# Performance work log

Measured on AMD Instinct MI355X. Metric: run time of the kernel, lower is better.

## Reference

```python
import jax, jax.numpy as jnp
import numpy as np
import math

B, C, H, W = 8, 512, 32, 32
ENC = 1024
L2 = 64
NH = 8
GROUPS = 32
EPS = 1e-5

def group_norm(x, gamma, beta):
    # x: (B, C, L) GroupNorm with 32 groups (float32)
    b, c, l = x.shape
    xg = x.reshape(b, GROUPS, (c // GROUPS) * l)
    mean = xg.mean(-1, keepdims=True)
    var = xg.var(-1, keepdims=True)
    xn = ((xg - mean) * jax.lax.rsqrt(var + EPS)).reshape(b, c, l)
    return xn * gamma[None, :, None] + beta[None, :, None]

def conv1x1(w, bias, x):
    # conv_nd(1, in, out, 1): w (out, in), x (B, in, L) -> (B, out, L)
    return jnp.einsum('oc,bcl->bol', w, x) + bias[None, :, None]

def setup_inputs() -> dict:
    key = jax.random.key(0)
    ks = jax.random.split(key, 16)
    s = lambda fan_in: 1.0 / math.sqrt(fan_in)
    inp = {
        'x': jax.random.normal(ks[0], (B, C, H, W), jnp.float32),
        'xf_out': jax.random.normal(ks[1], (B, ENC, L2), jnp.float32),
        'obj_class_embedding': jax.random.normal(ks[2], (B, ENC, L2), jnp.float32),
        'obj_bbox_embedding': jax.random.normal(ks[3], (B, ENC, L2), jnp.float32),
        'image_patch_bbox_embedding': jax.random.normal(ks[4], (B, ENC, H * W), jnp.float32),
        'key_padding_mask': jax.random.bernoulli(ks[5], 0.3, (B, L2)),
        'qkv_w': jax.random.normal(ks[6], (3 * C, C), jnp.float32) * s(C),
        'qkv_b': jnp.zeros((3 * C,), jnp.float32),
        'g_qkv': jnp.ones((C,), jnp.float32),
        'b_qkv': jnp.zeros((C,), jnp.float32),
        'lc_w': jax.random.normal(ks[7], (2 * C, ENC), jnp.float32) * s(ENC),
        'lc_b': jnp.zeros((2 * C,), jnp.float32),
        'lp_w': jax.random.normal(ks[8], (C, ENC), jnp.float32) * s(ENC),
        'lp_b': jnp.zeros((C,), jnp.float32),
        'g_obj': jnp.ones((ENC,), jnp.float32),
        'b_obj': jnp.zeros((ENC,), jnp.float32),
        'g_lpos': jnp.ones((C,), jnp.float32),
        'b_lpos': jnp.zeros((C,), jnp.float32),
        'g_ipos': jnp.ones((C,), jnp.float32),
        'b_ipos': jnp.zeros((C,), jnp.float32),
        # proj_out is zero-initialized in the original (zero_module); use random
        # weights so the projection math is exercised non-trivially.
        'proj_w': jax.random.normal(ks[9], (C, C), jnp.float32) * s(C),
        'proj_b': jnp.zeros((C,), jnp.float32),
    }
    return inp

def reference(x, xf_out, obj_class_embedding, obj_bbox_embedding,
              image_patch_bbox_embedding, key_padding_mask,
              qkv_w, qkv_b, g_qkv, b_qkv, lc_w, lc_b, lp_w, lp_b,
              g_obj, b_obj, g_lpos, b_lpos, g_ipos, b_ipos, proj_w, proj_b):
    b, c, h, w = x.shape
    L1 = h * w
    d = C // NH
    xf = x.reshape(b, c, L1)

    qkv = conv1x1(qkv_w, qkv_b, group_norm(xf, g_qkv, b_qkv))  # (B, 3C, L1)
    q, k, v = jnp.split(qkv, 3, axis=1)
    q = q.reshape(b * NH, d, L1)
    k = k.reshape(b * NH, d, L1)
    v = v.reshape(b * NH, d, L1)

    ipp = group_norm(conv1x1(lp_w, lp_b, image_patch_bbox_embedding), g_ipos, b_ipos)
    ipp = ipp.reshape(b * NH, d, L1)

    q_img = jnp.concatenate([q, ipp], axis=1)  # (B*H, 2d, L1)
    k_img = jnp.concatenate([k, ipp], axis=1)

    lpe = group_norm(conv1x1(lp_w, lp_b, obj_bbox_embedding), g_lpos, b_lpos)
    lpe = lpe.reshape(b * NH, d, L2)

    lce = (xf_out + group_norm(obj_class_embedding, g_obj, b_obj)) / 2
    kl, vl = jnp.split(conv1x1(lc_w, lc_b, lce), 2, axis=1)
    kl = kl.reshape(b * NH, d, L2)
    vl = vl.reshape(b * NH, d, L2)
    k_layout = jnp.concatenate([kl, lpe], axis=1)  # (B*H, 2d, L2)

    k_mix = jnp.concatenate([k_img, k_layout], axis=2)  # (B*H, 2d, L1+L2)
    v_mix = jnp.concatenate([v, vl], axis=2)             # (B*H, d, L1+L2)

    mask = jnp.concatenate([jnp.zeros((b, L1), bool), key_padding_mask], axis=1)  # (B, L1+L2)

    scale = 1.0 / math.sqrt(math.sqrt(2 * C // NH))
    attn = jnp.einsum('bct,bcs->bts', q_img * scale, k_mix * scale)  # (B*H, L1, L1+L2)
    attn = attn.reshape(b, NH, L1, L1 + L2)
    attn = jnp.where(mask[:, None, None, :], -jnp.inf, attn)
    attn = jax.nn.softmax(attn.astype(jnp.float32), axis=-1).astype(attn.dtype)
    attn = attn.reshape(b * NH, L1, L1 + L2)

    out = jnp.einsum('bts,bcs->bct', attn, v_mix).reshape(b, C, L1)
    hproj = conv1x1(proj_w, proj_b, out)
    return (xf + hproj).reshape(b, c, h, w)
```

## Files before the change

kernel.cpp:

```cpp
#include <hip/hip_runtime.h>
#include <math.h>

#define NB 8
#define NC 512
#define NL1 1024
#define NL2 64
#define NLKV 1088
#define NENC 1024
#define EPSV 1e-5f
#define SCALE2 0.08838834764831845f
#define SCALE2Q 0.12752425f
#define DEFER_THR 11.5415603f

typedef _Float16 half8 __attribute__((ext_vector_type(8)));
typedef _Float16 half4 __attribute__((ext_vector_type(4)));
typedef __fp16 fp16x2 __attribute__((ext_vector_type(2)));
typedef float f32x4 __attribute__((ext_vector_type(4)));
typedef float f32x16 __attribute__((ext_vector_type(16)));
typedef unsigned int uint32x2 __attribute__((ext_vector_type(2)));

__device__ __forceinline__ void gload16(const _Float16* g, _Float16* l) {
  __builtin_amdgcn_global_load_lds(
      (const __attribute__((address_space(1))) void*)g,
      (__attribute__((address_space(3))) void*)l, 16, 0, 0);
}

__device__ __forceinline__ unsigned int pkrtz(float a, float b) {
  union { fp16x2 hh; unsigned int uu; } cv;
  cv.hh = __builtin_amdgcn_cvt_pkrtz(a, b);
  return cv.uu;
}

__device__ __forceinline__ float fast_exp2(float x) {
  return __builtin_amdgcn_exp2f(x);
}

__global__ __launch_bounds__(256) void k_init(
    const float* __restrict__ x, const float* __restrict__ obj,
    float* __restrict__ xm, float* __restrict__ xr,
    float* __restrict__ om, float* __restrict__ orr,
    const float* __restrict__ qkv_w, _Float16* __restrict__ w16qkv,
    const float* __restrict__ lp_w, _Float16* __restrict__ w16lp,
    const float* __restrict__ proj_w, _Float16* __restrict__ w16proj,
    const float* __restrict__ lc_w, _Float16* __restrict__ w16lc)
{
  int bid = blockIdx.x;
  if (bid < 512) {
    const float* p; float* meanp; float* rstdp; int n4, n, bg;
    if (bid < 256) {
      bg = bid;
      int b = bg >> 5, g = bg & 31;
      p = x + ((size_t)b * 512 + (size_t)g * 16) * 1024;
      n = 16 * 1024; meanp = xm; rstdp = xr;
    } else {
      bg = bid - 256;
      int b = bg >> 5, g = bg & 31;
      p = obj + ((size_t)b * 1024 + (size_t)g * 32) * 64;
      n = 32 * 64; meanp = om; rstdp = orr;
    }
    n4 = n >> 2;
    float s = 0.f, s2 = 0.f;
    for (int i = threadIdx.x; i < n4; i += 256) {
      float4 v = ((const float4*)p)[i];
      s += v.x + v.y + v.z + v.w;
      s2 += v.x * v.x + v.y * v.y + v.z * v.z + v.w * v.w;
    }
    #pragma unroll
    for (int o = 32; o > 0; o >>= 1) { s += __shfl_down(s, o); s2 += __shfl_down(s2, o); }
    __shared__ float rs[4], rq[4];
    int lane = threadIdx.x & 63, w = threadIdx.x >> 6;
    if (lane == 0) { rs[w] = s; rq[w] = s2; }
    __syncthreads();
    if (threadIdx.x == 0) {
      float S = rs[0] + rs[1] + rs[2] + rs[3];
      float Q = rq[0] + rq[1] + rq[2] + rq[3];
      float m = S / n;
      float v = Q / n - m * m;
      if (v < 0.f) v = 0.f;
      meanp[bg] = m;
      rstdp[bg] = rsqrtf(v + EPSV);
    }
  } else {
    int cb = bid - 512;
    const float* s; _Float16* d; int i4;
    if (cb < 768)        { s = qkv_w;  d = w16qkv;  i4 = cb * 256 + threadIdx.x; }
    else if (cb < 1280)  { s = lp_w;   d = w16lp;   i4 = (cb - 768) * 256 + threadIdx.x; }
    else if (cb < 1536)  { s = proj_w; d = w16proj; i4 = (cb - 1280) * 256 + threadIdx.x; }
    else                 { s = lc_w;   d = w16lc;   i4 = (cb - 1536) * 256 + threadIdx.x; }
    float4 v = *(const float4*)&s[(size_t)i4 * 4];
    half4 o; o.x = (_Float16)v.x; o.y = (_Float16)v.y; o.z = (_Float16)v.z; o.w = (_Float16)v.w;
    *(half4*)&d[(size_t)i4 * 4] = o;
  }
}

__global__ __launch_bounds__(256) void k_prep(
    const float* __restrict__ x, const float* __restrict__ xm, const float* __restrict__ xr,
    const float* __restrict__ g_qkv, const float* __restrict__ b_qkv, _Float16* __restrict__ xT,
    const float* __restrict__ ipbe, _Float16* __restrict__ ipbeT,
    const float* __restrict__ xf_out, const float* __restrict__ obj_class,
    const float* __restrict__ obj_bbox,
    const float* __restrict__ om, const float* __restrict__ orr,
    const float* __restrict__ g_obj, const float* __restrict__ b_obj,
    _Float16* __restrict__ lceT, _Float16* __restrict__ objT)
{
  __shared__ _Float16 tile[64][72];
  const int bid = blockIdx.x;
  const int tl = threadIdx.x & 63;
  if (bid < 1024) {
    const int tt = bid & 15, ct = (bid >> 4) & 7, b = bid >> 7;
    const int c0 = ct * 64, t0 = tt * 64;
    const int cp = threadIdx.x >> 6;
    #pragma unroll
    for (int i = 0; i < 16; i++) {
      int c = c0 + i * 4 + cp;
      float v = x[((size_t)b * NC + c) * NL1 + t0 + tl];
      int g = c >> 4;
      float ga = g_qkv[c] * xr[b * 32 + g];
      float be = b_qkv[c] - xm[b * 32 + g] * ga;
      tile[tl][i * 4 + cp] = (_Float16)(v * ga + be);
    }
    __syncthreads();
    int tr = threadIdx.x >> 2, c16 = (threadIdx.x & 3) * 16;
    _Float16* dst = xT + ((size_t)b * 1024 + t0 + tr) * 512 + c0 + c16;
    *(half8*)dst = *(half8*)&tile[tr][c16];
    *(half8*)(dst + 8) = *(half8*)&tile[tr][c16 + 8];
  } else if (bid < 3072) {
    const int e2 = bid - 1024;
    const int tt = e2 & 15, et = (e2 >> 4) & 15, b = e2 >> 8;
    const int e0 = et * 64, t0 = tt * 64;
    const int ep = threadIdx.x >> 6;
    #pragma unroll
    for (int i = 0; i < 16; i++) {
      int e = e0 + i * 4 + ep;
      tile[tl][i * 4 + ep] = (_Float16)ipbe[((size_t)b * 1024 + e) * 1024 + t0 + tl];
    }
    __syncthreads();
    int tr = threadIdx.x >> 2, c16 = (threadIdx.x & 3) * 16;
    _Float16* d = ipbeT + ((size_t)b * 1024 + t0 + tr) * 1024 + e0 + c16;
    *(half8*)d = *(half8*)&tile[tr][c16];
    *(half8*)(d + 8) = *(half8*)&tile[tr][c16 + 8];
  } else {
    const int e2 = bid - 3072;
    const int et = e2 & 15, which = (e2 >> 4) & 1, b = e2 >> 5;
    const int e0 = et * 64;
    const int ep = threadIdx.x >> 6;
    if (which == 0) {
      #pragma unroll
      for (int i = 0; i < 16; i++) {
        int e = e0 + i * 4 + ep;
        size_t idx = ((size_t)b * 1024 + e) * 64 + tl;
        int g = e >> 5;
        float xn = (obj_class[idx] - om[b * 32 + g]) * orr[b * 32 + g] * g_obj[e] + b_obj[e];
        tile[tl][i * 4 + ep] = (_Float16)(0.5f * (xf_out[idx] + xn));
      }
    } else {
      #pragma unroll
      for (int i = 0; i < 16; i++) {
        int e = e0 + i * 4 + ep;
        tile[tl][i * 4 + ep] = (_Float16)obj_bbox[((size_t)b * 1024 + e) * 64 + tl];
      }
    }
    __syncthreads();
    int tr = threadIdx.x >> 2, c16 = (threadIdx.x & 3) * 16;
    _Float16* dst = (which == 0 ? lceT : objT) + ((size_t)b * 64 + tr) * 1024 + e0 + c16;
    *(half8*)dst = *(half8*)&tile[tr][c16];
    *(half8*)(dst + 8) = *(half8*)&tile[tr][c16 + 8];
  }
}

#define MFMA_CORE(KTOT)                                                                  \
  f32x4 acc[4][4];                                                                       \
  _Pragma("unroll") for (int i_ = 0; i_ < 4; i_++)                                       \
      _Pragma("unroll") for (int j_ = 0; j_ < 4; j_++) acc[i_][j_] = (f32x4)0.f;         \
  {                                                                                      \
    const int rsub = lane >> 3, csrc = (lane & 7) ^ rsub;                                \
    const int NT_ = (KTOT) / 64;                                                         \
    _Pragma("unroll") for (int i = 0; i < 4; i++) {                                      \
      int seg = w * 4 + i;                                                               \
      int row = seg * 8 + rsub;                                                          \
      gload16(Abase + (size_t)(m0 + row) * (KTOT) + csrc * 8, ldsA + seg * 512);         \
      gload16(Bbase + (size_t)(n0 + row) * (KTOT) + csrc * 8, ldsB + seg * 512);         \
    }                                                                                    \
    int cur_ = 0;                                                                        \
    for (int t_ = 0; t_ < NT_; t_++) {                                                   \
      if (t_ + 1 < NT_) {                                                                \
        _Float16* da_ = ldsA + ((cur_ ^ 1) << 13);                                       \
        _Float16* db_ = ldsB + ((cur_ ^ 1) << 13);                                       \
        int kt = (t_ + 1) * 64;                                                          \
        _Pragma("unroll") for (int i = 0; i < 4; i++) {                                  \
          int seg = w * 4 + i;                                                           \
          int row = seg * 8 + rsub;                                                      \
          gload16(Abase + (size_t)(m0 + row) * (KTOT) + kt + csrc * 8, da_ + seg * 512); \
          gload16(Bbase + (size_t)(n0 + row) * (KTOT) + kt + csrc * 8, db_ + seg * 512); \
        }                                                                                \
        asm volatile("s_waitcnt vmcnt(8)" ::: "memory");                                 \
      } else {                                                                           \
        asm volatile("s_waitcnt vmcnt(0)" ::: "memory");                                 \
      }                                                                                  \
      __builtin_amdgcn_s_barrier();                                                      \
      const char* ra_ = (const char*)(ldsA + (cur_ << 13));                              \
      const char* rb_ = (const char*)(ldsB + (cur_ << 13));                              \
      _Pragma("unroll") for (int kk = 0; kk < 2; kk++) {                                 \
        half8 af[4], bf[4];                                                              \
        _Pragma("unroll") for (int mb = 0; mb < 4; mb++) {                               \
          int row = wm + mb * 16 + l15;                                                  \
          af[mb] = *(const half8*)(ra_ + row * 128 +                                     \
                                   ((kk * 64 + lg * 16) ^ ((row & 7) << 4)));            \
        }                                                                                \
        _Pragma("unroll") for (int nb = 0; nb < 4; nb++) {                               \
          int row = wn + nb * 16 + l15;                                                  \
          bf[nb] = *(const half8*)(rb_ + row * 128 +                                     \
                                   ((kk * 64 + lg * 16) ^ ((row & 7) << 4)));            \
        }                                                                                \
        _Pragma("unroll") for (int mb = 0; mb < 4; mb++)                                 \
            _Pragma("unroll") for (int nb = 0; nb < 4; nb++)                             \
                acc[mb][nb] = __builtin_amdgcn_mfma_f32_16x16x32_f16(af[mb], bf[nb],     \
                                                                    acc[mb][nb], 0, 0, 0);\
      }                                                                                  \
      __builtin_amdgcn_s_barrier();                                                      \
      cur_ ^= 1;                                                                         \
    }                                                                                    \
  }

#define MFMA_CORE_N64(KTOT)                                                              \
  f32x4 acc[4][2];                                                                       \
  _Pragma("unroll") for (int i_ = 0; i_ < 4; i_++)                                       \
      _Pragma("unroll") for (int j_ = 0; j_ < 2; j_++) acc[i_][j_] = (f32x4)0.f;         \
  {                                                                                      \
    const int rsub = lane >> 3, csrc = (lane & 7) ^ rsub;                                \
    const int NT_ = (KTOT) / 64;                                                         \
    _Pragma("unroll") for (int i = 0; i < 4; i++) {                                      \
      int seg = w * 4 + i;                                                               \
      int row = seg * 8 + rsub;                                                          \
      gload16(Abase + (size_t)(m0 + row) * (KTOT) + csrc * 8, ldsA + seg * 512);         \
    }                                                                                    \
    _Pragma("unroll") for (int i = 0; i < 2; i++) {                                      \
      int seg = w * 2 + i;                                                               \
      int row = seg * 8 + rsub;                                                          \
      gload16(Bbase + (size_t)row * (KTOT) + csrc * 8, ldsB + seg * 512);                \
    }                                                                                    \
    int cur_ = 0;                                                                        \
    for (int t_ = 0; t_ < NT_; t_++) {                                                   \
      if (t_ + 1 < NT_) {                                                                \
        _Float16* da_ = ldsA + ((cur_ ^ 1) << 13);                                       \
        _Float16* db_ = ldsB + ((cur_ ^ 1) << 12);                                       \
        int kt = (t_ + 1) * 64;                                                          \
        _Pragma("unroll") for (int i = 0; i < 4; i++) {                                  \
          int seg = w * 4 + i;                                                           \
          int row = seg * 8 + rsub;                                                      \
          gload16(Abase + (size_t)(m0 + row) * (KTOT) + kt + csrc * 8, da_ + seg * 512); \
        }                                                                                \
        _Pragma("unroll") for (int i = 0; i < 2; i++) {                                  \
          int seg = w * 2 + i;                                                           \
          int row = seg * 8 + rsub;                                                      \
          gload16(Bbase + (size_t)row * (KTOT) + kt + csrc * 8, db_ + seg * 512);        \
        }                                                                                \
        asm volatile("s_waitcnt vmcnt(6)" ::: "memory");                                 \
      } else {                                                                           \
        asm volatile("s_waitcnt vmcnt(0)" ::: "memory");                                 \
      }                                                                                  \
      __builtin_amdgcn_s_barrier();                                                      \
      const char* ra_ = (const char*)(ldsA + (cur_ << 13));                              \
      const char* rb_ = (const char*)(ldsB + (cur_ << 12));                              \
      _Pragma("unroll") for (int kk = 0; kk < 2; kk++) {                                 \
        half8 af[4], bf[2];                                                              \
        _Pragma("unroll") for (int mb = 0; mb < 4; mb++) {                               \
          int row = wm + mb * 16 + l15;                                                  \
          af[mb] = *(const half8*)(ra_ + row * 128 +                                     \
                                   ((kk * 64 + lg * 16) ^ ((row & 7) << 4)));            \
        }                                                                                \
        _Pragma("unroll") for (int nb = 0; nb < 2; nb++) {                               \
          int row = wn + nb * 16 + l15;                                                  \
          bf[nb] = *(const half8*)(rb_ + row * 128 +                                     \
                                   ((kk * 64 + lg * 16) ^ ((row & 7) << 4)));            \
        }                                                                                \
        _Pragma("unroll") for (int mb = 0; mb < 4; mb++)                                 \
            _Pragma("unroll") for (int nb = 0; nb < 2; nb++)                             \
                acc[mb][nb] = __builtin_amdgcn_mfma_f32_16x16x32_f16(af[mb], bf[nb],     \
                                                                    acc[mb][nb], 0, 0, 0);\
      }                                                                                  \
      __builtin_amdgcn_s_barrier();                                                      \
      cur_ ^= 1;                                                                         \
    }                                                                                    \
  }

__global__ __launch_bounds__(256) void k_mfma_big(
    const _Float16* __restrict__ w16qkv, const float* __restrict__ qkv_b,
    const _Float16* __restrict__ xhatT,
    const _Float16* __restrict__ w16lp, const float* __restrict__ lp_b,
    const _Float16* __restrict__ ipbeT,
    const _Float16* __restrict__ w16lc, const float* __restrict__ lc_b,
    const _Float16* __restrict__ lceT, const _Float16* __restrict__ objT,
    const float* __restrict__ g_lpos, const float* __restrict__ b_lpos,
    _Float16* __restrict__ qT, _Float16* __restrict__ kT, _Float16* __restrict__ vT,
    _Float16* __restrict__ ipp16)
{
  __shared__ _Float16 smem[32768];
  const int bid0 = blockIdx.x;
  const int tid = threadIdx.x, lane = tid & 63, w = tid >> 6;
  const int l15 = lane & 15, lg = lane >> 4;

  if (bid0 < 256) {
    const int nt = bid0 & 7, mt = (bid0 >> 3) & 3, b = bid0 >> 5;
    const int m0 = mt * 128, n0 = nt * 128;
    _Float16* ldsA = smem;
    _Float16* ldsB = smem + 16384;
    const _Float16* Abase = w16lp;
    const _Float16* Bbase = ipbeT + (size_t)b * 1024 * 1024;
    const int wm = (w >> 1) * 64, wn = (w & 1) * 64;
    MFMA_CORE(1024)
    #pragma unroll
    for (int mb = 0; mb < 4; mb++) {
      #pragma unroll
      for (int r = 0; r < 4; r++) {
        int m = m0 + wm + mb * 16 + lg * 4 + r;
        float bia = lp_b[m];
        #pragma unroll
        for (int nb = 0; nb < 4; nb++) {
          int t = n0 + wn + nb * 16 + l15;
          ipp16[((size_t)b * NC + m) * NL1 + t] = (_Float16)(acc[mb][nb][r] + bia);
        }
      }
    }
  } else if (bid0 < 352) {
    const int local = bid0 - 256;
    const int mt = local % 12, b = local / 12;
    const bool islc = (mt < 8);
    const int m0 = (islc ? mt : mt - 8) * 128;
    _Float16* ldsA = smem;
    _Float16* ldsB = smem + 16384;
    float (*red_s)[4] = (float(*)[4])(smem + 24576);
    float (*red_q)[4] = (float(*)[4])(smem + 24608);
    const _Float16* Abase = islc ? w16lc : w16lp;
    const float* bias = islc ? lc_b : lp_b;
    const _Float16* Bbase = (islc ? lceT : objT) + (size_t)b * 64 * 1024;
    const int wm = (w >> 1) * 64, wn = (w & 1) * 32;
    MFMA_CORE_N64(1024)

    if (islc) {
      #pragma unroll
      for (int mb = 0; mb < 4; mb++) {
        #pragma unroll
        for (int r = 0; r < 4; r++) {
          int m = m0 + wm + mb * 16 + lg * 4 + r;
          float bia = bias[m];
          #pragma unroll
          for (int nb = 0; nb < 2; nb++) {
            int l = wn + nb * 16 + l15;
            float val = acc[mb][nb][r] + bia;
            if (m < 512) {
              int h = m >> 6, dc = m & 63;
              kT[(((size_t)b * 8 + h) * 1088 + 1024 + l) * 128 + dc] = (_Float16)val;
            } else {
              int mv = m - 512, h = mv >> 6, dc = mv & 63;
              vT[(((size_t)b * 8 + h) * 64 + dc) * 1088 + 1024 + l] = (_Float16)val;
            }
          }
        }
      }
    } else {
      float vals[4][2][4];
      float ps[4], pq[4];
      #pragma unroll
      for (int mb = 0; mb < 4; mb++) {
        ps[mb] = 0.f; pq[mb] = 0.f;
        #pragma unroll
        for (int r = 0; r < 4; r++) {
          int m = m0 + wm + mb * 16 + lg * 4 + r;
          float bia = bias[m];
          #pragma unroll
          for (int nb = 0; nb < 2; nb++) {
            float val = acc[mb][nb][r] + bia;
            vals[mb][nb][r] = val;
            ps[mb] += val; pq[mb] += val * val;
          }
        }
      }
      #pragma unroll
      for (int mb = 0; mb < 4; mb++) {
        #pragma unroll
        for (int o = 32; o > 0; o >>= 1) {
          ps[mb] += __shfl_xor(ps[mb], o);
          pq[mb] += __shfl_xor(pq[mb], o);
        }
      }
      if (lane == 0) {
        #pragma unroll
        for (int mb = 0; mb < 4; mb++) { red_s[w][mb] = ps[mb]; red_q[w][mb] = pq[mb]; }
      }
      __syncthreads();
      const int wbase = (wm >> 6) * 2;
      #pragma unroll
      for (int mb = 0; mb < 4; mb++) {
        float S = red_s[wbase][mb] + red_s[wbase + 1][mb];
        float Q = red_q[wbase][mb] + red_q[wbase + 1][mb];
        float mean = S * (1.f / 1024.f);
        float var = Q * (1.f / 1024.f) - mean * mean;
        if (var < 0.f) var = 0.f;
        float rstd = rsqrtf(var + EPSV);
        #pragma unroll
        for (int r = 0; r < 4; r++) {
          int c = m0 + wm + mb * 16 + lg * 4 + r;
          float ga = g_lpos[c] * rstd;
          float be = b_lpos[c] - mean * ga;
          int hh = c >> 6, dc = c & 63;
          #pragma unroll
          for (int nb = 0; nb < 2; nb++) {
            int l = wn + nb * 16 + l15;
            float xn = vals[mb][nb][r] * ga + be;
            kT[(((size_t)b * 8 + hh) * 1088 + 1024 + l) * 128 + 64 + dc] = (_Float16)xn;
          }
        }
      }
    }
  } else {
    const int bid = bid0 - 352;
    const int nt = bid & 7, tt = bid >> 3;
    const int mt = tt % 12, b = tt / 12;
    const int m0 = mt * 128, n0 = nt * 128;
    _Float16* ldsA = smem;
    _Float16* ldsB = smem + 16384;
    const _Float16* Abase = w16qkv;
    const _Float16* Bbase = xhatT + (size_t)b * 1024 * 512;
    const int wm = (w >> 1) * 64, wn = (w & 1) * 64;
    MFMA_CORE(512)

    char* tb = (char*)smem;
    if (m0 < 1024) {
      const bool isq = (m0 < 512);
      const float qs = isq ? SCALE2Q : 1.f;
      #pragma unroll
      for (int mb = 0; mb < 4; mb++) {
        #pragma unroll
        for (int r = 0; r < 4; r++) {
          int mcol = wm + mb * 16 + lg * 4 + r;
          float bia = qkv_b[m0 + mcol];
          #pragma unroll
          for (int nb = 0; nb < 4; nb++) {
            int trow = wn + nb * 16 + l15;
            float val = (acc[mb][nb][r] + bia) * qs;
            *(_Float16*)(tb + ((trow * 256 + mcol * 2) ^ ((trow & 7) << 4))) = (_Float16)val;
          }
        }
      }
      __syncthreads();
      #pragma unroll
      for (int it = 0; it < 8; it++) {
        int e = it * 256 + tid;
        int trow = e >> 4, seg = e & 15;
        half8 v = *(const half8*)(tb + ((trow * 256 + seg * 16) ^ ((trow & 7) << 4)));
        if (isq) {
          int mq = m0 + seg * 8, hh = mq >> 6, dc = mq & 63;
          *(half8*)(qT + (((size_t)b * 8 + hh) * 1024 + n0 + trow) * 128 + dc) = v;
        } else {
          int mk = m0 - 512 + seg * 8, hh = mk >> 6, dc = mk & 63;
          *(half8*)(kT + (((size_t)b * 8 + hh) * 1088 + n0 + trow) * 128 + dc) = v;
        }
      }
    } else {
      #pragma unroll
      for (int mb = 0; mb < 4; mb++) {
        #pragma unroll
        for (int r = 0; r < 4; r++) {
          int mrow = wm + mb * 16 + lg * 4 + r;
          float bia = qkv_b[m0 + mrow];
          #pragma unroll
          for (int nb = 0; nb < 4; nb++) {
            int tcol = wn + nb * 16 + l15;
            *(_Float16*)(tb + ((mrow * 256 + tcol * 2) ^ ((mrow & 7) << 4))) =
                (_Float16)(acc[mb][nb][r] + bia);
          }
        }
      }
      __syncthreads();
      #pragma unroll
      for (int it = 0; it < 8; it++) {
        int e = it * 256 + tid;
        int mrow = e >> 4, seg = e & 15;
        half8 v = *(const half8*)(tb + ((mrow * 256 + seg * 16) ^ ((mrow & 7) << 4)));
        int mv = m0 - 1024 + mrow, hh = mv >> 6, dc = mv & 63;
        *(half8*)(vT + (((size_t)b * 8 + hh) * 64 + dc) * 1088 + n0 + seg * 8) = v;
      }
    }
  }
}

__global__ __launch_bounds__(256) void k_mfma_proj(
    const _Float16* __restrict__ Abase, const float* __restrict__ bias,
    const _Float16* __restrict__ Ball, const float* __restrict__ xin,
    float* __restrict__ out)
{
  __shared__ _Float16 smem[32768];
  _Float16* ldsA = smem;
  _Float16* ldsB = smem + 16384;
  const int b = blockIdx.z, mt = blockIdx.y, nt = blockIdx.x;
  const int m0 = mt * 128, n0 = nt * 128;
  const _Float16* Bbase = Ball + (size_t)b * 1024 * 512;
  const int tid = threadIdx.x, lane = tid & 63, w = tid >> 6;
  const int l15 = lane & 15, lg = lane >> 4;
  const int wm = (w >> 1) * 64, wn = (w & 1) * 64;
  MFMA_CORE(512)
  #pragma unroll
  for (int mb = 0; mb < 4; mb++) {
    #pragma unroll
    for (int r = 0; r < 4; r++) {
      int m = m0 + wm + mb * 16 + lg * 4 + r;
      float bia = bias[m];
      #pragma unroll
      for (int nb = 0; nb < 4; nb++) {
        int t = n0 + wn + nb * 16 + l15;
        size_t idx = ((size_t)b * NC + m) * NL1 + t;
        out[idx] = xin[idx] + acc[mb][nb][r] + bia;
      }
    }
  }
}

__global__ __launch_bounds__(256) void k_ipp_fuse(
    const _Float16* __restrict__ raw,
    const float* __restrict__ gm, const float* __restrict__ gb,
    _Float16* __restrict__ qT, _Float16* __restrict__ kT)
{
  const int g = blockIdx.x, b = blockIdx.y;
  const int tid = threadIdx.x;
  const _Float16* p = raw + ((size_t)b * 512 + (size_t)g * 16) * 1024;
  const int t0 = tid * 4;

  float4 v[16];
  float s = 0.f, s2 = 0.f;
  #pragma unroll
  for (int c = 0; c < 16; c++) {
    half4 hv = *(const half4*)&p[(size_t)c * 1024 + t0];
    v[c].x = (float)hv.x; v[c].y = (float)hv.y; v[c].z = (float)hv.z; v[c].w = (float)hv.w;
    s += v[c].x + v[c].y + v[c].z + v[c].w;
    s2 += v[c].x * v[c].x + v[c].y * v[c].y + v[c].z * v[c].z + v[c].w * v[c].w;
  }
  #pragma unroll
  for (int o = 32; o > 0; o >>= 1) { s += __shfl_down(s, o); s2 += __shfl_down(s2, o); }
  __shared__ float rs[4], rq[4], stat[2];
  int lane = tid & 63, w = tid >> 6;
  if (lane == 0) { rs[w] = s; rq[w] = s2; }
  __syncthreads();
  if (tid == 0) {
    float S = rs[0] + rs[1] + rs[2] + rs[3];
    float Q = rq[0] + rq[1] + rq[2] + rq[3];
    float mn = S / 16384.f;
    float var = Q / 16384.f - mn * mn;
    if (var < 0.f) var = 0.f;
    stat[0] = mn; stat[1] = rsqrtf(var + EPSV);
  }
  __syncthreads();
  const float mn = stat[0], rstd = stat[1];

  float ga[16], be[16];
  #pragma unroll
  for (int c = 0; c < 16; c++) {
    ga[c] = gm[g * 16 + c] * rstd;
    be[c] = gb[g * 16 + c] - mn * ga[c];
  }

  const size_t bh = (size_t)b * 8 + (g >> 2);
  const int dcb = (g & 3) * 16;
  #pragma unroll
  for (int j = 0; j < 4; j++) {
    const int t = t0 + j;
    half8 k0, k1, q0, q1;
    #pragma unroll
    for (int c = 0; c < 8; c++) {
      float4 vc = v[c];
      float e = (j == 0) ? vc.x : (j == 1) ? vc.y : (j == 2) ? vc.z : vc.w;
      float xn = e * ga[c] + be[c];
      k0[c] = (_Float16)xn;
      q0[c] = (_Float16)(SCALE2Q * xn);
    }
    #pragma unroll
    for (int c = 8; c < 16; c++) {
      float4 vc = v[c];
      float e = (j == 0) ? vc.x : (j == 1) ? vc.y : (j == 2) ? vc.z : vc.w;
      float xn = e * ga[c] + be[c];
      k1[c - 8] = (_Float16)xn;
      q1[c - 8] = (_Float16)(SCALE2Q * xn);
    }
    _Float16* qd = qT + (bh * 1024 + t) * 128 + 64 + dcb;
    _Float16* kd = kT + (bh * 1088 + t) * 128 + 64 + dcb;
    *(half8*)qd = q0; *(half8*)(qd + 8) = q1;
    *(half8*)kd = k0; *(half8*)(kd + 8) = k1;
  }
}

__global__ __launch_bounds__(512, 1) void k_attn_mfma(
    const _Float16* __restrict__ qT, const _Float16* __restrict__ kT,
    const _Float16* __restrict__ vT, const int* __restrict__ mask,
    _Float16* __restrict__ attnT)
{
  const int bid = blockIdx.x;
  const int bh = bid & 63;
  const int qt = bid >> 6;
  const int b = bh >> 3, h = bh & 7;
  const int tid = threadIdx.x;
  const int lane = tid & 63;
  const int w = tid >> 6;
  const int l31 = lane & 31;
  const int hi = lane >> 5;

  __shared__ _Float16 KsB[2 * 64 * 128];
  __shared__ _Float16 VtB[3 * 64 * 64];

  const int q = qt * 256 + w * 32 + l31;

  half8 aq[8];
  {
    const _Float16* qp = qT + ((size_t)bh * 1024 + q) * 128 + hi * 8;
    #pragma unroll
    for (int kst = 0; kst < 8; kst++) aq[kst] = *(const half8*)(qp + kst * 16);
  }

  unsigned int mbits = 0;
  {
    const int* mp = mask + b * 64;
    #pragma unroll
    for (int sb = 0; sb < 2; sb++) {
      #pragma unroll
      for (int reg = 0; reg < 16; reg++) {
        int s = sb * 32 + (reg & 3) + 8 * (reg >> 2) + 4 * hi;
        if (mp[s]) mbits |= 1u << (sb * 16 + reg);
      }
    }
  }

  f32x16 O0 = (f32x16)0.f, O1 = (f32x16)0.f;
  f32x16 scA0 = (f32x16)0.f, scA1 = (f32x16)0.f;
  f32x16 scB0 = (f32x16)0.f, scB1 = (f32x16)0.f;
  float m_run = -INFINITY, l_run = 0.f;

  const int kxor = (l31 & 7) << 4;
  const int ksrow_off = lane >> 4;
  const int kcsrc_base = lane & 15;
  const int vdc_off = lane >> 3;
  const int vcsrc_base = lane & 7;

#define STAGE_KV(T, KD, VD)                                                          \
  {                                                                                  \
    const int s0_ = (T) * 64;                                                        \
    _Pragma("unroll") for (int r = 0; r < 2; r++) {                                  \
      int seg = r * 8 + w;                                                           \
      int srow = seg * 4 + ksrow_off;                                                \
      int csrc = kcsrc_base ^ (srow & 7);                                            \
      gload16(kT + ((size_t)bh * 1088 + s0_ + srow) * 128 + csrc * 8, (KD) + seg * 512); \
    }                                                                                \
    {                                                                                \
      int seg = w;                                                                   \
      int dc = seg * 8 + vdc_off;                                                    \
      int csrc = vcsrc_base ^ (dc & 7);                                              \
      gload16(vT + ((size_t)bh * 64 + dc) * 1088 + s0_ + csrc * 8, (VD) + seg * 512);  \
    }                                                                                \
  }

#define XHALF_FMAX(OUTV, INV)                                                        \
  { unsigned int xi_ = __float_as_uint(INV);                                         \
    uint32x2 xr_ = __builtin_amdgcn_permlane32_swap(xi_, xi_, false, false);         \
    OUTV = fmaxf(__uint_as_float(xr_.x), __uint_as_float(xr_.y)); }
#define XHALF_ADD(OUTV, INV)                                                         \
  { unsigned int xi_ = __float_as_uint(INV);                                         \
    uint32x2 xr_ = __builtin_amdgcn_permlane32_swap(xi_, xi_, false, false);         \
    OUTV = __uint_as_float(xr_.x) + __uint_as_float(xr_.y); }

#define ATTN_ITER(C0, C1, P0, P1, T)                                                 \
  {                                                                                  \
    const int T_ = (T);                                                              \
    if (T_ <= 16) {                                                                  \
      if (T_ <= 15) {                                                                \
        _Float16* kd_ = KsB + (((T_ + 1) & 1) << 13);                                \
        _Float16* vd_ = VtB + ((T_ + 1) % 3) * 4096;                                 \
        STAGE_KV(T_ + 1, kd_, vd_)                                                   \
      }                                                                              \
      const char* ksb_ = (const char*)(KsB + ((T_ & 1) << 13));                      \
      C0 = (f32x16)0.f; C1 = (f32x16)0.f;                                            \
      __builtin_amdgcn_s_setprio(1);                                                 \
      _Pragma("unroll") for (int kst = 0; kst < 8; kst++) {                          \
        half8 kf0 = *(const half8*)(ksb_ + ((l31 * 256 + kst * 32 + hi * 16) ^ kxor)); \
        half8 kf1 = *(const half8*)(ksb_ + (((32 + l31) * 256 + kst * 32 + hi * 16) ^ kxor)); \
        C0 = __builtin_amdgcn_mfma_f32_32x32x16_f16(kf0, aq[kst], C0, 0, 0, 0);      \
        C1 = __builtin_amdgcn_mfma_f32_32x32x16_f16(kf1, aq[kst], C1, 0, 0, 0);      \
      }                                                                              \
      __builtin_amdgcn_s_setprio(0);                                                 \
    }                                                                                \
    if (T_ >= 1) {                                                                   \
      if (T_ == 17) {                                                                \
        _Pragma("unroll") for (int i = 0; i < 16; i++) {                             \
          if ((mbits >> i) & 1)        P0[i] = -INFINITY;                            \
          if ((mbits >> (16 + i)) & 1) P1[i] = -INFINITY;                            \
        }                                                                            \
      }                                                                              \
      float mx;                                                                      \
      {                                                                              \
        float a0 = fmaxf(fmaxf(P0[0], P0[1]), P0[2]);                                \
        float a1 = fmaxf(fmaxf(P0[3], P0[4]), P0[5]);                                \
        float a2 = fmaxf(fmaxf(P0[6], P0[7]), P0[8]);                                \
        float a3 = fmaxf(fmaxf(P0[9], P0[10]), P0[11]);                              \
        float a4 = fmaxf(fmaxf(P0[12], P0[13]), P0[14]);                             \
        float a5 = fmaxf(fmaxf(P0[15], P1[0]), P1[1]);                               \
        float a6 = fmaxf(fmaxf(P1[2], P1[3]), P1[4]);                                \
        float a7 = fmaxf(fmaxf(P1[5], P1[6]), P1[7]);                                \
        float a8 = fmaxf(fmaxf(P1[8], P1[9]), P1[10]);                               \
        float a9 = fmaxf(fmaxf(P1[11], P1[12]), P1[13]);                             \
        float aa = fmaxf(P1[14], P1[15]);                                            \
        float b0 = fmaxf(fmaxf(a0, a1), a2);                                         \
        float b1 = fmaxf(fmaxf(a3, a4), a5);                                         \
        float b2 = fmaxf(fmaxf(a6, a7), a8);                                         \
        float b3 = fmaxf(a9, aa);                                                    \
        mx = fmaxf(fmaxf(b0, b1), fmaxf(b2, b3));                                    \
      }                                                                              \
      XHALF_FMAX(mx, mx)                                                             \
      if (__all(mx <= m_run + DEFER_THR)) {                                          \
        float sum = 0.f;                                                             \
        _Pragma("unroll") for (int i = 0; i < 16; i++) {                             \
          float p = fast_exp2(P0[i] - m_run); P0[i] = p; sum += p; }                 \
        _Pragma("unroll") for (int i = 0; i < 16; i++) {                             \
          float p = fast_exp2(P1[i] - m_run); P1[i] = p; sum += p; }                 \
        XHALF_ADD(sum, sum)                                                          \
        l_run += sum;                                                                \
      } else {                                                                       \
        float m_new = fmaxf(m_run, mx);                                              \
        float alpha = fast_exp2(m_run - m_new);                                      \
        float sum = 0.f;                                                             \
        _Pragma("unroll") for (int i = 0; i < 16; i++) {                             \
          float p = fast_exp2(P0[i] - m_new); P0[i] = p; sum += p; }                 \
        _Pragma("unroll") for (int i = 0; i < 16; i++) {                             \
          float p = fast_exp2(P1[i] - m_new); P1[i] = p; sum += p; }                 \
        XHALF_ADD(sum, sum)                                                          \
        l_run = l_run * alpha + sum;                                                 \
        m_run = m_new;                                                               \
        _Pragma("unroll") for (int i = 0; i < 16; i++) { O0[i] *= alpha; O1[i] *= alpha; } \
      }                                                                              \
      const char* vtb_ = (const char*)(VtB + ((T_ - 1) % 3) * 4096);                 \
      __builtin_amdgcn_s_setprio(1);                                                 \
      _Pragma("unroll") for (int sb = 0; sb < 2; sb++) {                             \
        _Pragma("unroll") for (int k2 = 0; k2 < 2; k2++) {                           \
          const int kst = sb * 2 + k2;                                               \
          unsigned int pa0, pa1, pb0, pb1;                                           \
          if (sb == 0) {                                                             \
            pa0 = pkrtz(P0[8 * k2 + 0], P0[8 * k2 + 1]);                             \
            pa1 = pkrtz(P0[8 * k2 + 2], P0[8 * k2 + 3]);                             \
            pb0 = pkrtz(P0[8 * k2 + 4], P0[8 * k2 + 5]);                             \
            pb1 = pkrtz(P0[8 * k2 + 6], P0[8 * k2 + 7]);                             \
          } else {                                                                   \
            pa0 = pkrtz(P1[8 * k2 + 0], P1[8 * k2 + 1]);                             \
            pa1 = pkrtz(P1[8 * k2 + 2], P1[8 * k2 + 3]);                             \
            pb0 = pkrtz(P1[8 * k2 + 4], P1[8 * k2 + 5]);                             \
            pb1 = pkrtz(P1[8 * k2 + 6], P1[8 * k2 + 7]);                             \
          }                                                                          \
          uint32x2 r0_ = __builtin_amdgcn_permlane32_swap(pa0, pb0, false, false);   \
          uint32x2 r1_ = __builtin_amdgcn_permlane32_swap(pa1, pb1, false, false);   \
          union { unsigned int u[4]; half8 hh; } pf;                                 \
          pf.u[0] = r0_.x;                                                           \
          pf.u[1] = r1_.x;                                                           \
          pf.u[2] = r0_.y;                                                           \
          pf.u[3] = r1_.y;                                                           \
          half8 vf0 = *(const half8*)(vtb_ + ((l31 * 128 + kst * 32 + hi * 16) ^ kxor)); \
          half8 vf1 = *(const half8*)(vtb_ + (((32 + l31) * 128 + kst * 32 + hi * 16) ^ kxor)); \
          O0 = __builtin_amdgcn_mfma_f32_32x32x16_f16(vf0, pf.hh, O0, 0, 0, 0);      \
          O1 = __builtin_amdgcn_mfma_f32_32x32x16_f16(vf1, pf.hh, O1, 0, 0, 0);      \
        }                                                                            \
      }                                                                              \
      __builtin_amdgcn_s_setprio(0);                                                 \
    }                                                                                \
    if (T_ < 17) {                                                                   \
      asm volatile("s_waitcnt vmcnt(0)" ::: "memory");                               \
      __builtin_amdgcn_s_barrier();                                                  \
    }                                                                                \
  }

  STAGE_KV(0, KsB, VtB)
  asm volatile("s_waitcnt vmcnt(0)" ::: "memory");
  __builtin_amdgcn_s_barrier();

  for (int t = 0; t < 18; t += 2) {
    ATTN_ITER(scA0, scA1, scB0, scB1, t)
    ATTN_ITER(scB0, scB1, scA0, scA1, t + 1)
  }

  float inv = 1.f / l_run;
  _Float16* op = attnT + ((size_t)b * 1024 + q) * 512 + h * 64;
  #pragma unroll
  for (int i = 0; i < 16; i += 2) {
    int dc = (i & 3) + 8 * (i >> 2) + 4 * hi;
    unsigned int c0 = pkrtz(O0[i] * inv, O0[i + 1] * inv);
    unsigned int c1 = pkrtz(O1[i] * inv, O1[i + 1] * inv);
    *(unsigned int*)(op + dc) = c0;
    *(unsigned int*)(op + 32 + dc) = c1;
  }
}

extern "C" void kernel_launch(void* const* d_in, const int* in_sizes, int n_in,
                              void* d_out, int out_size, void* d_ws, size_t ws_size,
                              hipStream_t stream) {
  const float* x         = (const float*)d_in[0];
  const float* xf_out    = (const float*)d_in[1];
  const float* obj_class = (const float*)d_in[2];
  const float* obj_bbox  = (const float*)d_in[3];
  const float* ipbe      = (const float*)d_in[4];
  const int*   mask      = (const int*)d_in[5];
  const float* qkv_w     = (const float*)d_in[6];
  const float* qkv_b     = (const float*)d_in[7];
  const float* g_qkv     = (const float*)d_in[8];
  const float* b_qkv     = (const float*)d_in[9];
  const float* lc_w      = (const float*)d_in[10];
  const float* lc_b      = (const float*)d_in[11];
  const float* lp_w      = (const float*)d_in[12];
  const float* lp_b      = (const float*)d_in[13];
  const float* g_obj     = (const float*)d_in[14];
  const float* b_obj     = (const float*)d_in[15];
  const float* g_lpos    = (const float*)d_in[16];
  const float* b_lpos    = (const float*)d_in[17];
  const float* g_ipos    = (const float*)d_in[18];
  const float* b_ipos    = (const float*)d_in[19];
  const float* proj_w    = (const float*)d_in[20];
  const float* proj_b    = (const float*)d_in[21];
  float* out = (float*)d_out;

  _Float16* f16b = (_Float16*)d_ws;
  _Float16* qT      = f16b;
  _Float16* kT      = qT + 8388608;
  _Float16* vT      = kT + 8912896;
  _Float16* xhatT   = vT + 4456448;
  _Float16* ipbeT   = xhatT + 4194304;
  _Float16* attnT   = ipbeT + 8388608;
  _Float16* w16qkv  = attnT + 4194304;
  _Float16* w16lp   = w16qkv + 786432;
  _Float16* w16proj = w16lp + 524288;
  _Float16* w16lc   = w16proj + 262144;
  _Float16* lceT    = w16lc + 1048576;
  _Float16* objT    = lceT + 524288;
  _Float16* ipp16   = objT + 524288;
  float* st = (float*)(ipp16 + 4194304);
  float* xm = st, * xr = st + 256, * om = st + 512, * orr = st + 768;

  dim3 blk(256);
  k_init<<<dim3(3072), blk, 0, stream>>>(x, obj_class, xm, xr, om, orr,
                                         qkv_w, w16qkv, lp_w, w16lp, proj_w, w16proj, lc_w, w16lc);
  k_prep<<<dim3(3328), blk, 0, stream>>>(x, xm, xr, g_qkv, b_qkv, xhatT,
                                         ipbe, ipbeT,
                                         xf_out, obj_class, obj_bbox, om, orr, g_obj, b_obj,
                                         lceT, objT);
  k_mfma_big<<<dim3(1120), blk, 0, stream>>>(w16qkv, qkv_b, xhatT,
                                             w16lp, lp_b, ipbeT,
                                             w16lc, lc_b, lceT, objT,
                                             g_lpos, b_lpos,
                                             qT, kT, vT, ipp16);
  k_ipp_fuse<<<dim3(32, 8), blk, 0, stream>>>(ipp16, g_ipos, b_ipos, qT, kT);
  k_attn_mfma<<<dim3(256), dim3(512), 0, stream>>>(qT, kT, vT, mask, attnT);
  k_mfma_proj<<<dim3(8, 4, 8), blk, 0, stream>>>(w16proj, proj_b, attnT, x, out);
}
```

Baseline: 125.5 us.

## Enlarge big GEMM tiles to 256x256 with 512-thread blocks

The fused projection GEMM kernel moves from 128x128 tiles with 256 threads to 256x256 tiles with 512 threads and 128KB of LDS, cutting the grid from 1120 to 304 blocks. The small N=64 GEMMs pair two 128-row tiles per block, using the two halves of the block. Larger tiles raise operand reuse per LDS load and reduce redundant global reads. In exchange, each block uses more LDS and registers, and the epilogue transpose goes through two serialized passes with extra barriers. Fewer blocks may also leave some of the device's compute units idle.

```diff
diff --git a/kernel.cpp b/kernel.cpp
--- a/kernel.cpp
+++ b/kernel.cpp
@@ -168,9 +168,9 @@
   }
 }
 
-#define MFMA_CORE(KTOT)                                                                  \
-  f32x4 acc[4][4];                                                                       \
-  _Pragma("unroll") for (int i_ = 0; i_ < 4; i_++)                                       \
+#define MFMA_CORE_256(KTOT)                                                              \
+  f32x4 acc[8][4];                                                                       \
+  _Pragma("unroll") for (int i_ = 0; i_ < 8; i_++)                                       \
       _Pragma("unroll") for (int j_ = 0; j_ < 4; j_++) acc[i_][j_] = (f32x4)0.f;         \
   {                                                                                      \
     const int rsub = lane >> 3, csrc = (lane & 7) ^ rsub;                                \
@@ -184,8 +184,8 @@
     int cur_ = 0;                                                                        \
     for (int t_ = 0; t_ < NT_; t_++) {                                                   \
       if (t_ + 1 < NT_) {                                                                \
-        _Float16* da_ = ldsA + ((cur_ ^ 1) << 13);                                       \
-        _Float16* db_ = ldsB + ((cur_ ^ 1) << 13);                                       \
+        _Float16* da_ = ldsA + ((cur_ ^ 1) << 14);                                       \
+        _Float16* db_ = ldsB + ((cur_ ^ 1) << 14);                                       \
         int kt = (t_ + 1) * 64;                                                          \
         _Pragma("unroll") for (int i = 0; i < 4; i++) {                                  \
           int seg = w * 4 + i;                                                           \
@@ -198,11 +198,11 @@
         asm volatile("s_waitcnt vmcnt(0)" ::: "memory");                                 \
       }                                                                                  \
       __builtin_amdgcn_s_barrier();                                                      \
-      const char* ra_ = (const char*)(ldsA + (cur_ << 13));                              \
-      const char* rb_ = (const char*)(ldsB + (cur_ << 13));                              \
+      const char* ra_ = (const char*)(ldsA + (cur_ << 14));                              \
+      const char* rb_ = (const char*)(ldsB + (cur_ << 14));                              \
       _Pragma("unroll") for (int kk = 0; kk < 2; kk++) {                                 \
-        half8 af[4], bf[4];                                                              \
-        _Pragma("unroll") for (int mb = 0; mb < 4; mb++) {                               \
+        half8 af[8], bf[4];                                                              \
+        _Pragma("unroll") for (int mb = 0; mb < 8; mb++) {                               \
           int row = wm + mb * 16 + l15;                                                  \
           af[mb] = *(const half8*)(ra_ + row * 128 +                                     \
                                    ((kk * 64 + lg * 16) ^ ((row & 7) << 4)));            \
@@ -212,7 +212,7 @@
           bf[nb] = *(const half8*)(rb_ + row * 128 +                                     \
                                    ((kk * 64 + lg * 16) ^ ((row & 7) << 4)));            \
         }                                                                                \
-        _Pragma("unroll") for (int mb = 0; mb < 4; mb++)                                 \
+        _Pragma("unroll") for (int mb = 0; mb < 8; mb++)                                 \
             _Pragma("unroll") for (int nb = 0; nb < 4; nb++)                             \
                 acc[mb][nb] = __builtin_amdgcn_mfma_f32_16x16x32_f16(af[mb], bf[nb],     \
                                                                     acc[mb][nb], 0, 0, 0);\
@@ -284,7 +284,61 @@
     }                                                                                    \
   }
 
-__global__ __launch_bounds__(256) void k_mfma_big(
+#define MFMA_CORE(KTOT)                                                                  \
+  f32x4 acc[4][4];                                                                       \
+  _Pragma("unroll") for (int i_ = 0; i_ < 4; i_++)                                       \
+      _Pragma("unroll") for (int j_ = 0; j_ < 4; j_++) acc[i_][j_] = (f32x4)0.f;         \
+  {                                                                                      \
+    const int rsub = lane >> 3, csrc = (lane & 7) ^ rsub;                                \
+    const int NT_ = (KTOT) / 64;                                                         \
+    _Pragma("unroll") for (int i = 0; i < 4; i++) {                                      \
+      int seg = w * 4 + i;                                                               \
+      int row = seg * 8 + rsub;                                                          \
+      gload16(Abase + (size_t)(m0 + row) * (KTOT) + csrc * 8, ldsA + seg * 512);         \
+      gload16(Bbase + (size_t)(n0 + row) * (KTOT) + csrc * 8, ldsB + seg * 512);         \
+    }                                                                                    \
+    int cur_ = 0;                                                                        \
+    for (int t_ = 0; t_ < NT_; t_++) {                                                   \
+      if (t_ + 1 < NT_) {                                                                \
+        _Float16* da_ = ldsA + ((cur_ ^ 1) << 13);                                       \
+        _Float16* db_ = ldsB + ((cur_ ^ 1) << 13);                                       \
+        int kt = (t_ + 1) * 64;                                                          \
+        _Pragma("unroll") for (int i = 0; i < 4; i++) {                                  \
+          int seg = w * 4 + i;                                                           \
+          int row = seg * 8 + rsub;                                                      \
+          gload16(Abase + (size_t)(m0 + row) * (KTOT) + kt + csrc * 8, da_ + seg * 512); \
+          gload16(Bbase + (size_t)(n0 + row) * (KTOT) + kt + csrc * 8, db_ + seg * 512); \
+        }                                                                                \
+        asm volatile("s_waitcnt vmcnt(8)" ::: "memory");                                 \
+      } else {                                                                           \
+        asm volatile("s_waitcnt vmcnt(0)" ::: "memory");                                 \
+      }                                                                                  \
+      __builtin_amdgcn_s_barrier();                                                      \
+      const char* ra_ = (const char*)(ldsA + (cur_ << 13));                              \
+      const char* rb_ = (const char*)(ldsB + (cur_ << 13));                              \
+      _Pragma("unroll") for (int kk = 0; kk < 2; kk++) {                                 \
+        half8 af[4], bf[4];                                                              \
+        _Pragma("unroll") for (int mb = 0; mb < 4; mb++) {                               \
+          int row = wm + mb * 16 + l15;                                                  \
+          af[mb] = *(const half8*)(ra_ + row * 128 +                                     \
+                                   ((kk * 64 + lg * 16) ^ ((row & 7) << 4)));            \
+        }                                                                                \
+        _Pragma("unroll") for (int nb = 0; nb < 4; nb++) {                               \
+          int row = wn + nb * 16 + l15;                                                  \
+          bf[nb] = *(const half8*)(rb_ + row * 128 +                                     \
+                                   ((kk * 64 + lg * 16) ^ ((row & 7) << 4)));            \
+        }                                                                                \
+        _Pragma("unroll") for (int mb = 0; mb < 4; mb++)                                 \
+            _Pragma("unroll") for (int nb = 0; nb < 4; nb++)                             \
+                acc[mb][nb] = __builtin_amdgcn_mfma_f32_16x16x32_f16(af[mb], bf[nb],     \
+                                                                    acc[mb][nb], 0, 0, 0);\
+      }                                                                                  \
+      __builtin_amdgcn_s_barrier();                                                      \
+      cur_ ^= 1;                                                                         \
+    }                                                                                    \
+  }
+
+__global__ __launch_bounds__(512, 2) void k_mfma_big(
     const _Float16* __restrict__ w16qkv, const float* __restrict__ qkv_b,
     const _Float16* __restrict__ xhatT,
     const _Float16* __restrict__ w16lp, const float* __restrict__ lp_b,
@@ -295,22 +349,22 @@
     _Float16* __restrict__ qT, _Float16* __restrict__ kT, _Float16* __restrict__ vT,
     _Float16* __restrict__ ipp16)
 {
-  __shared__ _Float16 smem[32768];
+  __shared__ _Float16 smem[65536];
   const int bid0 = blockIdx.x;
   const int tid = threadIdx.x, lane = tid & 63, w = tid >> 6;
-  const int l15 = lane & 15, lg = lane >> 4;
-
-  if (bid0 < 256) {
-    const int nt = bid0 & 7, mt = (bid0 >> 3) & 3, b = bid0 >> 5;
-    const int m0 = mt * 128, n0 = nt * 128;
+  const int l15 = lane & 15, lg = (lane >> 4) & 3;
+
+  if (bid0 < 64) {
+    const int nt = bid0 & 3, mt = (bid0 >> 2) & 1, b = bid0 >> 3;
+    const int m0 = mt * 256, n0 = nt * 256;
     _Float16* ldsA = smem;
-    _Float16* ldsB = smem + 16384;
+    _Float16* ldsB = smem + 32768;
     const _Float16* Abase = w16lp;
     const _Float16* Bbase = ipbeT + (size_t)b * 1024 * 1024;
-    const int wm = (w >> 1) * 64, wn = (w & 1) * 64;
-    MFMA_CORE(1024)
+    const int wm = (w >> 2) * 128, wn = (w & 3) * 64;
+    MFMA_CORE_256(1024)
     #pragma unroll
-    for (int mb = 0; mb < 4; mb++) {
+    for (int mb = 0; mb < 8; mb++) {
       #pragma unroll
       for (int r = 0; r < 4; r++) {
         int m = m0 + wm + mb * 16 + lg * 4 + r;
@@ -322,164 +376,197 @@
         }
       }
     }
-  } else if (bid0 < 352) {
-    const int local = bid0 - 256;
-    const int mt = local % 12, b = local / 12;
-    const bool islc = (mt < 8);
-    const int m0 = (islc ? mt : mt - 8) * 128;
-    _Float16* ldsA = smem;
-    _Float16* ldsB = smem + 16384;
-    float (*red_s)[4] = (float(*)[4])(smem + 24576);
-    float (*red_q)[4] = (float(*)[4])(smem + 24608);
+  } else if (bid0 < 112) {
+    const int local = bid0 - 64;
+    const int j = local % 6, b = local / 6;
+    const int h = w >> 2;
+    const bool islc = (j < 4);
+    const int m0 = islc ? (j * 2 + h) * 128 : ((j - 4) * 2 + h) * 128;
+    _Float16* ldsA = smem + h * 24576;
+    _Float16* ldsB = smem + h * 24576 + 16384;
+    float (*red_s)[4] = (float(*)[4])((char*)smem + 98304);
+    float (*red_q)[4] = (float(*)[4])((char*)smem + 98304 + 128);
     const _Float16* Abase = islc ? w16lc : w16lp;
     const float* bias = islc ? lc_b : lp_b;
     const _Float16* Bbase = (islc ? lceT : objT) + (size_t)b * 64 * 1024;
-    const int wm = (w >> 1) * 64, wn = (w & 1) * 32;
-    MFMA_CORE_N64(1024)
-
-    if (islc) {
-      #pragma unroll
-      for (int mb = 0; mb < 4; mb++) {
+    {
+      const int w = (tid >> 6) & 3;
+      const int wm = (w >> 1) * 64, wn = (w & 1) * 32;
+      MFMA_CORE_N64(1024)
+
+      if (islc) {
         #pragma unroll
-        for (int r = 0; r < 4; r++) {
-          int m = m0 + wm + mb * 16 + lg * 4 + r;
-          float bia = bias[m];
+        for (int mb = 0; mb < 4; mb++) {
           #pragma unroll
-          for (int nb = 0; nb < 2; nb++) {
-            int l = wn + nb * 16 + l15;
-            float val = acc[mb][nb][r] + bia;
-            if (m < 512) {
-              int h = m >> 6, dc = m & 63;
-              kT[(((size_t)b * 8 + h) * 1088 + 1024 + l) * 128 + dc] = (_Float16)val;
-            } else {
-              int mv = m - 512, h = mv >> 6, dc = mv & 63;
-              vT[(((size_t)b * 8 + h) * 64 + dc) * 1088 + 1024 + l] = (_Float16)val;
+          for (int r = 0; r < 4; r++) {
+            int m = m0 + wm + mb * 16 + lg * 4 + r;
+            float bia = bias[m];
+            #pragma unroll
+            for (int nb = 0; nb < 2; nb++) {
+              int l = wn + nb * 16 + l15;
+              float val = acc[mb][nb][r] + bia;
+              if (m < 512) {
+                int hh = m >> 6, dc = m & 63;
+                kT[(((size_t)b * 8 + hh) * 1088 + 1024 + l) * 128 + dc] = (_Float16)val;
+              } else {
+                int mv = m - 512, hh = mv >> 6, dc = mv & 63;
+                vT[(((size_t)b * 8 + hh) * 64 + dc) * 1088 + 1024 + l] = (_Float16)val;
+              }
+            }
+          }
+        }
+      } else {
+        float vals[4][2][4];
+        float ps[4], pq[4];
+        #pragma unroll
+        for (int mb = 0; mb < 4; mb++) {
+          ps[mb] = 0.f; pq[mb] = 0.f;
+          #pragma unroll
+          for (int r = 0; r < 4; r++) {
+            int m = m0 + wm + mb * 16 + lg * 4 + r;
+            float bia = bias[m];
+            #pragma unroll
+            for (int nb = 0; nb < 2; nb++) {
+              float val = acc[mb][nb][r] + bia;
+              vals[mb][nb][r] = val;
+              ps[mb] += val; pq[mb] += val * val;
+            }
+          }
+        }
+        #pragma unroll
+        for (int mb = 0; mb < 4; mb++) {
+          #pragma unroll
+          for (int o = 32; o > 0; o >>= 1) {
+            ps[mb] += __shfl_xor(ps[mb], o);
+            pq[mb] += __shfl_xor(pq[mb], o);
+          }
+        }
+        if (lane == 0) {
+          #pragma unroll
+          for (int mb = 0; mb < 4; mb++) { red_s[h * 4 + w][mb] = ps[mb]; red_q[h * 4 + w][mb] = pq[mb]; }
+        }
+        __syncthreads();
+        const int wbase = h * 4 + (wm >> 6) * 2;
+        #pragma unroll
+        for (int mb = 0; mb < 4; mb++) {
+          float S = red_s[wbase][mb] + red_s[wbase + 1][mb];
+          float Q = red_q[wbase][mb] + red_q[wbase + 1][mb];
+          float mean = S * (1.f / 1024.f);
+          float var = Q * (1.f / 1024.f) - mean * mean;
+          if (var < 0.f) var = 0.f;
+          float rstd = rsqrtf(var + EPSV);
+          #pragma unroll
+          for (int r = 0; r < 4; r++) {
+            int c = m0 + wm + mb * 16 + lg * 4 + r;
+            float ga = g_lpos[c] * rstd;
+            float be = b_lpos[c] - mean * ga;
+            int hh = c >> 6, dc = c & 63;
+            #pragma unroll
+            for (int nb = 0; nb < 2; nb++) {
+              int l = wn + nb * 16 + l15;
+              float xn = vals[mb][nb][r] * ga + be;
+              kT[(((size_t)b * 8 + hh) * 1088 + 1024 + l) * 128 + 64 + dc] = (_Float16)xn;
             }
           }
         }
       }
-    } else {
-      float vals[4][2][4];
-      float ps[4], pq[4];
-      #pragma unroll
-      for (int mb = 0; mb < 4; mb++) {
-        ps[mb] = 0.f; pq[mb] = 0.f;
-        #pragma unroll
-        for (int r = 0; r < 4; r++) {
-          int m = m0 + wm + mb * 16 + lg * 4 + r;
-          float bia = bias[m];
-          #pragma unroll
-          for (int nb = 0; nb < 2; nb++) {
-            float val = acc[mb][nb][r] + bia;
-            vals[mb][nb][r] = val;
-            ps[mb] += val; pq[mb] += val * val;
-          }
-        }
-      }
-      #pragma unroll
-      for (int mb = 0; mb < 4; mb++) {
-        #pragma unroll
-        for (int o = 32; o > 0; o >>= 1) {
-          ps[mb] += __shfl_xor(ps[mb], o);
-          pq[mb] += __shfl_xor(pq[mb], o);
-        }
-      }
-      if (lane == 0) {
-        #pragma unroll
-        for (int mb = 0; mb < 4; mb++) { red_s[w][mb] = ps[mb]; red_q[w][mb] = pq[mb]; }
-      }
-      __syncthreads();
-      const int wbase = (wm >> 6) * 2;
-      #pragma unroll
-      for (int mb = 0; mb < 4; mb++) {
-        float S = red_s[wbase][mb] + red_s[wbase + 1][mb];
-        float Q = red_q[wbase][mb] + red_q[wbase + 1][mb];
-        float mean = S * (1.f / 1024.f);
-        float var = Q * (1.f / 1024.f) - mean * mean;
-        if (var < 0.f) var = 0.f;
-        float rstd = rsqrtf(var + EPSV);
-        #pragma unroll
-        for (int r = 0; r < 4; r++) {
-          int c = m0 + wm + mb * 16 + lg * 4 + r;
-          float ga = g_lpos[c] * rstd;
-          float be = b_lpos[c] - mean * ga;
-          int hh = c >> 6, dc = c & 63;
-          #pragma unroll
-          for (int nb = 0; nb < 2; nb++) {
-            int l = wn + nb * 16 + l15;
-            float xn = vals[mb][nb][r] * ga + be;
-            kT[(((size_t)b * 8 + hh) * 1088 + 1024 + l) * 128 + 64 + dc] = (_Float16)xn;
-          }
-        }
-      }
     }
   } else {
-    const int bid = bid0 - 352;
-    const int nt = bid & 7, tt = bid >> 3;
-    const int mt = tt % 12, b = tt / 12;
-    const int m0 = mt * 128, n0 = nt * 128;
+    const int local = bid0 - 112;
+    const int nt = local & 3, tt = local >> 2;
+    const int mt = tt % 6, b = tt / 6;
+    const int m0 = mt * 256, n0 = nt * 256;
     _Float16* ldsA = smem;
-    _Float16* ldsB = smem + 16384;
+    _Float16* ldsB = smem + 32768;
     const _Float16* Abase = w16qkv;
     const _Float16* Bbase = xhatT + (size_t)b * 1024 * 512;
-    const int wm = (w >> 1) * 64, wn = (w & 1) * 64;
-    MFMA_CORE(512)
+    const int wm = (w >> 2) * 128, wn = (w & 3) * 64;
+    MFMA_CORE_256(512)
 
     char* tb = (char*)smem;
+    const int mi_w = w >> 2;
+    const int ti_w = (w & 3) >> 1;
+    const int w1 = w & 1;
+
     if (m0 < 1024) {
       const bool isq = (m0 < 512);
       const float qs = isq ? SCALE2Q : 1.f;
       #pragma unroll
-      for (int mb = 0; mb < 4; mb++) {
-        #pragma unroll
-        for (int r = 0; r < 4; r++) {
-          int mcol = wm + mb * 16 + lg * 4 + r;
-          float bia = qkv_b[m0 + mcol];
+      for (int ti = 0; ti < 2; ti++) {
+        if (ti_w == ti) {
+          char* tbm = tb + mi_w * 32768;
           #pragma unroll
-          for (int nb = 0; nb < 4; nb++) {
-            int trow = wn + nb * 16 + l15;
-            float val = (acc[mb][nb][r] + bia) * qs;
-            *(_Float16*)(tb + ((trow * 256 + mcol * 2) ^ ((trow & 7) << 4))) = (_Float16)val;
+          for (int mb = 0; mb < 8; mb++) {
+            #pragma unroll
+            for (int r = 0; r < 4; r++) {
+              int mloc = mb * 16 + lg * 4 + r;
+              float bia = qkv_b[m0 + mi_w * 128 + mloc];
+              #pragma unroll
+              for (int nb = 0; nb < 4; nb++) {
+                int tloc = w1 * 64 + nb * 16 + l15;
+                float val = (acc[mb][nb][r] + bia) * qs;
+                *(_Float16*)(tbm + ((tloc * 256 + mloc * 2) ^ ((tloc & 7) << 4))) = (_Float16)val;
+              }
+            }
           }
         }
-      }
-      __syncthreads();
-      #pragma unroll
-      for (int it = 0; it < 8; it++) {
-        int e = it * 256 + tid;
-        int trow = e >> 4, seg = e & 15;
-        half8 v = *(const half8*)(tb + ((trow * 256 + seg * 16) ^ ((trow & 7) << 4)));
-        if (isq) {
-          int mq = m0 + seg * 8, hh = mq >> 6, dc = mq & 63;
-          *(half8*)(qT + (((size_t)b * 8 + hh) * 1024 + n0 + trow) * 128 + dc) = v;
-        } else {
-          int mk = m0 - 512 + seg * 8, hh = mk >> 6, dc = mk & 63;
-          *(half8*)(kT + (((size_t)b * 8 + hh) * 1088 + n0 + trow) * 128 + dc) = v;
+        __syncthreads();
+        #pragma unroll
+        for (int mi = 0; mi < 2; mi++) {
+          char* tbm = tb + mi * 32768;
+          #pragma unroll
+          for (int it = 0; it < 4; it++) {
+            int e = it * 512 + tid;
+            int trow = e >> 4, seg = e & 15;
+            half8 v = *(const half8*)(tbm + ((trow * 256 + seg * 16) ^ ((trow & 7) << 4)));
+            int t = n0 + ti * 128 + trow;
+            int mm = m0 + mi * 128 + seg * 8;
+            if (isq) {
+              int hh = mm >> 6, dc = mm & 63;
+              *(half8*)(qT + (((size_t)b * 8 + hh) * 1024 + t) * 128 + dc) = v;
+            } else {
+              int mk = mm - 512, hh = mk >> 6, dc = mk & 63;
+              *(half8*)(kT + (((size_t)b * 8 + hh) * 1088 + t) * 128 + dc) = v;
+            }
+          }
         }
+        __syncthreads();
       }
     } else {
       #pragma unroll
-      for (int mb = 0; mb < 4; mb++) {
-        #pragma unroll
-        for (int r = 0; r < 4; r++) {
-          int mrow = wm + mb * 16 + lg * 4 + r;
-          float bia = qkv_b[m0 + mrow];
+      for (int ti = 0; ti < 2; ti++) {
+        if (ti_w == ti) {
+          char* tbm = tb + mi_w * 32768;
           #pragma unroll
-          for (int nb = 0; nb < 4; nb++) {
-            int tcol = wn + nb * 16 + l15;
-            *(_Float16*)(tb + ((mrow * 256 + tcol * 2) ^ ((mrow & 7) << 4))) =
-                (_Float16)(acc[mb][nb][r] + bia);
+          for (int mb = 0; mb < 8; mb++) {
+            #pragma unroll
+            for (int r = 0; r < 4; r++) {
+              int mloc = mb * 16 + lg * 4 + r;
+              float bia = qkv_b[m0 + mi_w * 128 + mloc];
+              #pragma unroll
+              for (int nb = 0; nb < 4; nb++) {
+                int tloc = w1 * 64 + nb * 16 + l15;
+                *(_Float16*)(tbm + ((mloc * 256 + tloc * 2) ^ ((mloc & 7) << 4))) =
+                    (_Float16)(acc[mb][nb][r] + bia);
+              }
+            }
           }
         }
-      }
-      __syncthreads();
-      #pragma unroll
-      for (int it = 0; it < 8; it++) {
-        int e = it * 256 + tid;
-        int mrow = e >> 4, seg = e & 15;
-        half8 v = *(const half8*)(tb + ((mrow * 256 + seg * 16) ^ ((mrow & 7) << 4)));
-        int mv = m0 - 1024 + mrow, hh = mv >> 6, dc = mv & 63;
-        *(half8*)(vT + (((size_t)b * 8 + hh) * 64 + dc) * 1088 + n0 + seg * 8) = v;
+        __syncthreads();
+        #pragma unroll
+        for (int mi = 0; mi < 2; mi++) {
+          char* tbm = tb + mi * 32768;
+          #pragma unroll
+          for (int it = 0; it < 4; it++) {
+            int e = it * 512 + tid;
+            int mrow = e >> 4, seg = e & 15;
+            half8 v = *(const half8*)(tbm + ((mrow * 256 + seg * 16) ^ ((mrow & 7) << 4)));
+            int mv = m0 - 1024 + mi * 128 + mrow, hh = mv >> 6, dc = mv & 63;
+            int t = n0 + ti * 128 + seg * 8;
+            *(half8*)(vT + (((size_t)b * 8 + hh) * 64 + dc) * 1088 + t) = v;
+          }
+        }
+        __syncthreads();
       }
     }
   }
@@ -843,11 +930,11 @@
                                          ipbe, ipbeT,
                                          xf_out, obj_class, obj_bbox, om, orr, g_obj, b_obj,
                                          lceT, objT);
-  k_mfma_big<<<dim3(1120), blk, 0, stream>>>(w16qkv, qkv_b, xhatT,
-                                             w16lp, lp_b, ipbeT,
-                                             w16lc, lc_b, lceT, objT,
-                                             g_lpos, b_lpos,
-                                             qT, kT, vT, ipp16);
+  k_mfma_big<<<dim3(304), dim3(512), 0, stream>>>(w16qkv, qkv_b, xhatT,
+                                                  w16lp, lp_b, ipbeT,
+                                                  w16lc, lc_b, lceT, objT,
+                                                  g_lpos, b_lpos,
+                                                  qT, kT, vT, ipp16);
   k_ipp_fuse<<<dim3(32, 8), blk, 0, stream>>>(ipp16, g_ipos, b_ipos, qT, kT);
   k_attn_mfma<<<dim3(256), dim3(512), 0, stream>>>(qT, kT, vT, mask, attnT);
   k_mfma_proj<<<dim3(8, 4, 8), blk, 0, stream>>>(w16proj, proj_b, attnT, x, out);
```

After: 135.7 us. 8.1% more time.
